# Kernel tuning notes

Hardware: AMD Instinct MI355X
Metric: run time of the kernel (lower is better)

## Reference

```python
import itertools
import jax, jax.numpy as jnp
import numpy as np

B, S, DIM = 1024, 49, 448
KEY_DIM, NUM_HEADS, ATTN_RATIO, RES = 32, 8, 4, 7
EXP_DIM = ATTN_RATIO * KEY_DIM            # 128
TOT_KEY = KEY_DIM * NUM_HEADS             # 256
TOT_EXP = EXP_DIM * NUM_HEADS             # 1024
QKV_OUT = TOT_EXP + 2 * TOT_KEY           # 1536
MLP_HID = 4 * DIM                         # 1792
SCALE = KEY_DIM ** -0.5
LN_EPS = 1e-5


def _build_bias_idxs():
    points = list(itertools.product(range(RES), range(RES)))
    offsets = {}
    idxs = []
    for p1 in points:
        for p2 in points:
            off = (abs(p1[0] - p2[0]), abs(p1[1] - p2[1]))
            if off not in offsets:
                offsets[off] = len(offsets)
            idxs.append(offsets[off])
    return np.array(idxs, dtype=np.int32).reshape(len(points), len(points)), len(offsets)


def setup_inputs() -> dict:
    key = jax.random.key(0)
    ks = jax.random.split(key, 16)
    bias_idxs_np, n_off = _build_bias_idxs()
    sd = 0.02
    return {
        "hidden_states": jax.random.normal(ks[0], (B, S, DIM), jnp.float32),
        "qkv_w": jax.random.normal(ks[1], (DIM, QKV_OUT), jnp.float32) * sd,
        "qkv_b": jnp.zeros((QKV_OUT,), jnp.float32),
        "proj_w": jax.random.normal(ks[2], (TOT_EXP, DIM), jnp.float32) * sd,
        "proj_b": jnp.zeros((DIM,), jnp.float32),
        "ln1_g": jnp.ones((DIM,), jnp.float32),
        "ln1_b": jnp.zeros((DIM,), jnp.float32),
        "ln2_g": jnp.ones((DIM,), jnp.float32),
        "ln2_b": jnp.zeros((DIM,), jnp.float32),
        "mlp_w1": jax.random.normal(ks[3], (DIM, MLP_HID), jnp.float32) * sd,
        "mlp_b1": jnp.zeros((MLP_HID,), jnp.float32),
        "mlp_w2": jax.random.normal(ks[4], (MLP_HID, DIM), jnp.float32) * sd,
        "mlp_b2": jnp.zeros((DIM,), jnp.float32),
        "attn_biases": jax.random.normal(ks[5], (NUM_HEADS, n_off), jnp.float32) * sd,
        "ls1": jax.random.normal(ks[6], (DIM,), jnp.float32) * 0.1,
        "ls2": jax.random.normal(ks[7], (DIM,), jnp.float32) * 0.1,
        "bias_idxs": jnp.asarray(bias_idxs_np),
    }


def _layer_norm(x, g, b):
    mu = jnp.mean(x, axis=-1, keepdims=True)
    var = jnp.mean(jnp.square(x - mu), axis=-1, keepdims=True)
    return (x - mu) * jax.lax.rsqrt(var + LN_EPS) * g + b


def reference(hidden_states, qkv_w, qkv_b, proj_w, proj_b,
              ln1_g, ln1_b, ln2_g, ln2_b,
              mlp_w1, mlp_b1, mlp_w2, mlp_b2,
              attn_biases, ls1, ls2, bias_idxs):
    x = hidden_states
    h = _layer_norm(x, ln1_g, ln1_b)
    qkv = h @ qkv_w + qkv_b                               # [B,S,1536]
    qkv = qkv.reshape(B, S, NUM_HEADS, KEY_DIM * 2 + EXP_DIM)
    q, k, v = jnp.split(qkv, [KEY_DIM, 2 * KEY_DIM], axis=3)
    bias = attn_biases[:, bias_idxs]                      # [H,S,S]
    scores = jnp.einsum('bqhd,bkhd->bhqk', q, k) * SCALE + bias
    probs = jax.nn.softmax(scores, axis=-1)
    ctx = jnp.einsum('bhqk,bkhd->bqhd', probs, v).reshape(B, S, TOT_EXP)
    attn_out = ctx @ proj_w + proj_b                      # [B,S,DIM]
    x = x + ls1 * attn_out
    h2 = _layer_norm(x, ln2_g, ln2_b)
    m = jax.nn.gelu(h2 @ mlp_w1 + mlp_b1, approximate=False) @ mlp_w2 + mlp_b2
    return x + ls2 * m
```

## Files before the change

### kernel.cpp

```cpp
#include <hip/hip_runtime.h>
#include <hip/hip_bf16.h>
#include <cstdint>

typedef unsigned short u16;
typedef __bf16 bf16x8 __attribute__((ext_vector_type(8)));
typedef float f32x4 __attribute__((ext_vector_type(4)));

#define DEV __device__ __forceinline__

static constexpr int BATCH = 1024, SEQ = 49, DIM = 448;
static constexpr int NH = 8, DV = 128;
static constexpr int QKV_N = 1536, MLP_H = 1792;
static constexpr float SCALE = 0.17677669529663687f;

DEV u16 f2bf(float f) {
    uint32_t u = __builtin_bit_cast(uint32_t, f);
    u += 0x7fffu + ((u >> 16) & 1u);
    return (u16)(u >> 16);
}

DEV void gload16(const void* g, void* l) {
    __builtin_amdgcn_global_load_lds(
        (__attribute__((address_space(1))) void*)const_cast<void*>(g),
        (__attribute__((address_space(3))) void*)l, 16, 0, 0);
}

#define MFMA(a, b, c) __builtin_amdgcn_mfma_f32_16x16x32_bf16((a), (b), (c), 0, 0, 0)

__global__ __launch_bounds__(256) void transpose_cast(const float* __restrict__ src,
                                                      u16* __restrict__ dst,
                                                      int K, int N, int Npad) {
    __shared__ float t[32][33];
    int nbk = K >> 5;
    int bk = blockIdx.x % nbk;
    int bn = blockIdx.x / nbk;
    int lx = threadIdx.x & 31, ly = threadIdx.x >> 5;
    int n0 = bn * 32, k0 = bk * 32;
    #pragma unroll
    for (int i = 0; i < 32; i += 8) {
        int k = k0 + ly + i, n = n0 + lx;
        t[ly + i][lx] = (n < N) ? src[(size_t)k * N + n] : 0.f;
    }
    __syncthreads();
    #pragma unroll
    for (int i = 0; i < 32; i += 8) {
        int n = n0 + ly + i, k = k0 + lx;
        dst[(size_t)n * K + k] = f2bf(t[lx][ly + i]);
    }
}

__global__ void build_bias(const float* __restrict__ ab, const int* __restrict__ idxs,
                           float* __restrict__ tab, int n_off) {
    int i = blockIdx.x * 256 + threadIdx.x;
    if (i >= NH * 49 * 49) return;
    int h = i / 2401, rem = i % 2401;
    tab[i] = ab[h * n_off + idxs[rem]];
}

__global__ __launch_bounds__(256) void ln_kernel(const float* __restrict__ x,
                                                 const float* __restrict__ g,
                                                 const float* __restrict__ bb,
                                                 u16* __restrict__ out) {
    int row = blockIdx.x * 4 + (threadIdx.x >> 6);
    int l = threadIdx.x & 63;
    const float* xr = x + (size_t)row * DIM;
    float v[7];
    float s = 0.f;
    #pragma unroll
    for (int j = 0; j < 7; j++) { v[j] = xr[l + j * 64]; s += v[j]; }
    #pragma unroll
    for (int m = 32; m; m >>= 1) s += __shfl_xor(s, m, 64);
    float mu = s * (1.f / 448.f);
    float var = 0.f;
    #pragma unroll
    for (int j = 0; j < 7; j++) { float d = v[j] - mu; var += d * d; }
    #pragma unroll
    for (int m = 32; m; m >>= 1) var += __shfl_xor(var, m, 64);
    float rs = rsqrtf(var * (1.f / 448.f) + 1e-5f);
    u16* orow = out + (size_t)row * DIM;
    #pragma unroll
    for (int j = 0; j < 7; j++) {
        int c = l + j * 64;
        orow[c] = f2bf((v[j] - mu) * rs * g[c] + bb[c]);
    }
}

template <int EPI>
__global__ __launch_bounds__(512, 6) void gemm128(const u16* __restrict__ A,
                                                  const u16* __restrict__ BT,
                                                  int Mreal, int N, int K, int Nreal,
                                                  const float* __restrict__ bias,
                                                  const float* __restrict__ ls,
                                                  const float* __restrict__ xres,
                                                  u16* __restrict__ outB,
                                                  float* __restrict__ outF) {
    __shared__ __align__(16) u16 sa[128 * 64];
    __shared__ __align__(16) u16 sb[128 * 64];
    const int tid = threadIdx.x;
    const int tilesN = N >> 7;

    int bid = blockIdx.x;
    int nwg = gridDim.x;
    if ((nwg & 7) == 0) {
        int cpx = nwg >> 3;
        bid = (bid & 7) * cpx + (bid >> 3);
    }
    const int tm = bid / tilesN, tn = bid % tilesN;

    const int w = tid >> 6, l = tid & 63;
    const int wm = (w >> 2) * 64, wn = (w & 3) * 32;
    const int l15 = l & 15, l4 = l >> 4;

    const u16* gA[2];
    const u16* gB[2];
    int loff[2];
    const size_t baseB = (size_t)(tn * 128) * K;
    #pragma unroll
    for (int i = 0; i < 2; i++) {
        int lc = i * 512 + tid;
        int row = lc >> 3, cs = lc & 7;
        int scs = cs ^ (row & 7);
        int gm = tm * 128 + row;
        gm = gm < Mreal ? gm : Mreal - 1;
        gA[i] = A + (size_t)gm * K + scs * 8;
        gB[i] = BT + baseB + (size_t)row * K + scs * 8;
        loff[i] = (row * 8 + cs) * 8;
    }

    f32x4 acc[4][2];
    #pragma unroll
    for (int i = 0; i < 4; i++)
        #pragma unroll
        for (int j = 0; j < 2; j++) acc[i][j] = (f32x4){0.f, 0.f, 0.f, 0.f};

    const int nk = K >> 6;
    #pragma unroll 1
    for (int kt = 0; kt < nk; ++kt) {
        const int k0 = kt << 6;
        #pragma unroll
        for (int i = 0; i < 2; i++) gload16(gA[i] + k0, &sa[loff[i]]);
        #pragma unroll
        for (int i = 0; i < 2; i++) gload16(gB[i] + k0, &sb[loff[i]]);
        __syncthreads();
        #pragma unroll
        for (int ks = 0; ks < 2; ++ks) {
            bf16x8 af[4], bfr[2];
            #pragma unroll
            for (int i = 0; i < 4; i++) {
                int row = wm + i * 16 + l15;
                int c = (ks * 4 + l4) ^ (row & 7);
                af[i] = *(const bf16x8*)&sa[row * 64 + c * 8];
            }
            #pragma unroll
            for (int j = 0; j < 2; j++) {
                int row = wn + j * 16 + l15;
                int c = (ks * 4 + l4) ^ (row & 7);
                bfr[j] = *(const bf16x8*)&sb[row * 64 + c * 8];
            }
            #pragma unroll
            for (int i = 0; i < 4; i++)
                #pragma unroll
                for (int j = 0; j < 2; j++)
                    acc[i][j] = MFMA(af[i], bfr[j], acc[i][j]);
        }
        __syncthreads();
    }

    #pragma unroll
    for (int i = 0; i < 4; i++) {
        int row0 = tm * 128 + wm + i * 16 + l4 * 4;
        #pragma unroll
        for (int j = 0; j < 2; j++) {
            int col = tn * 128 + wn + j * 16 + l15;
            if (col >= Nreal) continue;
            float bv = bias[col];
            #pragma unroll
            for (int r = 0; r < 4; r++) {
                int m = row0 + r;
                if (m >= Mreal) continue;
                float v = acc[i][j][r] + bv;
                if (EPI == 0) {
                    outB[(size_t)m * Nreal + col] = f2bf(v);
                } else if (EPI == 1) {
                    float gl = 0.5f * v * (1.f + erff(v * 0.70710678118654752f));
                    outB[(size_t)m * Nreal + col] = f2bf(gl);
                } else {
                    outF[(size_t)m * DIM + col] = xres[(size_t)m * DIM + col] + ls[col] * v;
                }
            }
        }
    }
}

__global__ __launch_bounds__(256) void attn_kernel(const u16* __restrict__ qkv,
                                                   const float* __restrict__ btab,
                                                   u16* __restrict__ ctx) {
    __shared__ __align__(16) u16 sq[64 * 40];
    __shared__ __align__(16) u16 sk[64 * 40];
    __shared__ __align__(16) u16 sv[128 * 72];
    __shared__ __align__(16) u16 sp[64 * 72];
    const int tid = threadIdx.x;
    const int bh = blockIdx.x;
    const int b = bh >> 3, h = bh & 7;
    const int w = tid >> 6, l = tid & 63, l15 = l & 15, l4 = l >> 4;
    const f32x4 Z4 = {0.f, 0.f, 0.f, 0.f};
    const size_t rowbase = (size_t)(b * SEQ) * QKV_N + h * 192;

    for (int c = tid; c < SEQ * 4; c += 256) {
        int s = c >> 2, ch = c & 3;
        *(uint4*)&sq[s * 40 + ch * 8] = *(const uint4*)(qkv + rowbase + (size_t)s * QKV_N + ch * 8);
        *(uint4*)&sk[s * 40 + ch * 8] = *(const uint4*)(qkv + rowbase + (size_t)s * QKV_N + 32 + ch * 8);
    }
    for (int c = tid; c < 15 * 5; c += 256) {
        int s = SEQ + c / 5, ch = c % 5;
        *(uint4*)&sq[s * 40 + ch * 8] = (uint4){0, 0, 0, 0};
        *(uint4*)&sk[s * 40 + ch * 8] = (uint4){0, 0, 0, 0};
    }
    for (int c = tid; c < SEQ * 16; c += 256) {
        int s = c >> 4, ch = c & 15;
        uint4 vv = *(const uint4*)(qkv + rowbase + (size_t)s * QKV_N + 64 + ch * 8);
        const u16* pv = (const u16*)&vv;
        #pragma unroll
        for (int j = 0; j < 8; j++) sv[(ch * 8 + j) * 72 + s] = pv[j];
    }
    for (int c = tid; c < 128 * 15; c += 256) {
        int d = c / 15, s = SEQ + c % 15;
        sv[d * 72 + s] = 0;
    }
    __syncthreads();

    bf16x8 aq = *(const bf16x8*)&sq[(w * 16 + l15) * 40 + l4 * 8];
    f32x4 sc[4];
    #pragma unroll
    for (int j = 0; j < 4; j++) {
        bf16x8 bk = *(const bf16x8*)&sk[(j * 16 + l15) * 40 + l4 * 8];
        sc[j] = MFMA(aq, bk, Z4);
    }
    #pragma unroll
    for (int r = 0; r < 4; r++) {
        int row = w * 16 + l4 * 4 + r;
        float pv[4];
        #pragma unroll
        for (int j = 0; j < 4; j++) {
            int col = j * 16 + l15;
            float sval = -1e30f;
            if (row < SEQ && col < SEQ)
                sval = sc[j][r] * SCALE + btab[(h * SEQ + row) * SEQ + col];
            pv[j] = sval;
        }
        float m = fmaxf(fmaxf(pv[0], pv[1]), fmaxf(pv[2], pv[3]));
        #pragma unroll
        for (int mask = 1; mask < 16; mask <<= 1) m = fmaxf(m, __shfl_xor(m, mask, 16));
        float s = 0.f;
        #pragma unroll
        for (int j = 0; j < 4; j++) { pv[j] = expf(pv[j] - m); s += pv[j]; }
        #pragma unroll
        for (int mask = 1; mask < 16; mask <<= 1) s += __shfl_xor(s, mask, 16);
        float inv = 1.f / s;
        #pragma unroll
        for (int j = 0; j < 4; j++) sp[row * 72 + j * 16 + l15] = f2bf(pv[j] * inv);
    }
    __syncthreads();

    bf16x8 ap0 = *(const bf16x8*)&sp[(w * 16 + l15) * 72 + l4 * 8];
    bf16x8 ap1 = *(const bf16x8*)&sp[(w * 16 + l15) * 72 + 32 + l4 * 8];
    #pragma unroll
    for (int j = 0; j < 8; j++) {
        bf16x8 b0 = *(const bf16x8*)&sv[(j * 16 + l15) * 72 + l4 * 8];
        bf16x8 b1 = *(const bf16x8*)&sv[(j * 16 + l15) * 72 + 32 + l4 * 8];
        f32x4 a = MFMA(ap0, b0, Z4);
        a = MFMA(ap1, b1, a);
        #pragma unroll
        for (int r = 0; r < 4; r++) {
            int row = w * 16 + l4 * 4 + r;
            if (row < SEQ)
                ctx[((size_t)(b * SEQ) + row) * 1024 + h * DV + j * 16 + l15] = f2bf(a[r]);
        }
    }
}

extern "C" void kernel_launch(void* const* d_in, const int* in_sizes, int n_in,
                              void* d_out, int out_size, void* d_ws, size_t ws_size,
                              hipStream_t stream) {
    const float* x = (const float*)d_in[0];
    const float* qkv_w = (const float*)d_in[1];
    const float* qkv_b = (const float*)d_in[2];
    const float* proj_w = (const float*)d_in[3];
    const float* proj_b = (const float*)d_in[4];
    const float* ln1_g = (const float*)d_in[5];
    const float* ln1_b = (const float*)d_in[6];
    const float* ln2_g = (const float*)d_in[7];
    const float* ln2_b = (const float*)d_in[8];
    const float* mlp_w1 = (const float*)d_in[9];
    const float* mlp_b1 = (const float*)d_in[10];
    const float* mlp_w2 = (const float*)d_in[11];
    const float* mlp_b2 = (const float*)d_in[12];
    const float* attn_biases = (const float*)d_in[13];
    const float* ls1 = (const float*)d_in[14];
    const float* ls2 = (const float*)d_in[15];
    const int* bias_idxs = (const int*)d_in[16];
    int n_off = in_sizes[13] / NH;
    float* out = (float*)d_out;

    auto al = [](size_t b) { return (b + 255) & ~(size_t)255; };
    const size_t wbytes = al((size_t)QKV_N * DIM * 2) + al((size_t)512 * 1024 * 2) +
                          al((size_t)MLP_H * DIM * 2) + al((size_t)512 * MLP_H * 2) +
                          al((size_t)NH * 2401 * 4);

    int nc = 32;
    {
        const int cands[6] = {1, 2, 4, 8, 16, 32};
        for (int ci = 0; ci < 6; ci++) {
            size_t R = (size_t)(BATCH / cands[ci]) * SEQ;
            size_t need = wbytes + al(R * DIM * 2) + al(R * MLP_H * 2) + al(R * 1024 * 2);
            if (need <= ws_size) { nc = cands[ci]; break; }
        }
    }
    const int CH = BATCH / nc;
    const int R = CH * SEQ;
    const int MT = (R + 127) >> 7;

    char* ws = (char*)d_ws;
    size_t off = 0;
    auto alloc = [&](size_t bytes) {
        void* p = ws + off;
        off += al(bytes);
        return p;
    };
    u16* wt_qkv = (u16*)alloc((size_t)QKV_N * DIM * 2);
    u16* wt_proj = (u16*)alloc((size_t)512 * 1024 * 2);
    u16* wt_m1 = (u16*)alloc((size_t)MLP_H * DIM * 2);
    u16* wt_m2 = (u16*)alloc((size_t)512 * MLP_H * 2);
    float* btab = (float*)alloc((size_t)NH * 2401 * 4);
    u16* hbuf = (u16*)alloc((size_t)R * DIM * 2);
    u16* big = (u16*)alloc((size_t)R * MLP_H * 2);
    u16* ctx = (u16*)alloc((size_t)R * 1024 * 2);

    transpose_cast<<<(DIM / 32) * (QKV_N / 32), 256, 0, stream>>>(qkv_w, wt_qkv, DIM, QKV_N, QKV_N);
    transpose_cast<<<(1024 / 32) * (512 / 32), 256, 0, stream>>>(proj_w, wt_proj, 1024, DIM, 512);
    transpose_cast<<<(DIM / 32) * (MLP_H / 32), 256, 0, stream>>>(mlp_w1, wt_m1, DIM, MLP_H, MLP_H);
    transpose_cast<<<(MLP_H / 32) * (512 / 32), 256, 0, stream>>>(mlp_w2, wt_m2, MLP_H, DIM, 512);
    build_bias<<<(NH * 2401 + 255) / 256, 256, 0, stream>>>(attn_biases, bias_idxs, btab, n_off);

    for (int c = 0; c < nc; ++c) {
        const float* xc = x + (size_t)c * R * DIM;
        float* oc = out + (size_t)c * R * DIM;

        ln_kernel<<<R / 4, 256, 0, stream>>>(xc, ln1_g, ln1_b, hbuf);
        gemm128<0><<<MT * (QKV_N / 128), 512, 0, stream>>>(
            hbuf, wt_qkv, R, QKV_N, DIM, QKV_N, qkv_b, nullptr, nullptr, big, nullptr);
        attn_kernel<<<CH * NH, 256, 0, stream>>>(big, btab, ctx);
        gemm128<2><<<MT * 4, 512, 0, stream>>>(
            ctx, wt_proj, R, 512, 1024, DIM, proj_b, ls1, xc, nullptr, oc);
        ln_kernel<<<R / 4, 256, 0, stream>>>(oc, ln2_g, ln2_b, hbuf);
        gemm128<1><<<MT * (MLP_H / 128), 512, 0, stream>>>(
            hbuf, wt_m1, R, MLP_H, DIM, MLP_H, mlp_b1, nullptr, nullptr, big, nullptr);
        gemm128<2><<<MT * 4, 512, 0, stream>>>(
            big, wt_m2, R, 512, MLP_H, DIM, mlp_b2, ls2, oc, nullptr, oc);
    }
}
```

Measured before the change: 755.2 us.

## Double-buffer GEMM LDS tiles with prefetch two k-steps ahead

Splits the GEMM's shared-memory A/B tiles into two buffers and issues global-to-LDS loads for tile kt+2 while tile kt is being computed, using explicit vmcnt waits and barriers. The aim is to hide global load latency behind MFMA work instead of stalling on a sync every k-step. This doubles LDS use to 64KB per block, and the launch-bounds occupancy hint drops from 6 to 4 blocks.

```diff
diff --git a/kernel.cpp b/kernel.cpp
--- a/kernel.cpp
+++ b/kernel.cpp
@@ -86,7 +86,7 @@
 }
 
 template <int EPI>
-__global__ __launch_bounds__(512, 6) void gemm128(const u16* __restrict__ A,
+__global__ __launch_bounds__(512, 4) void gemm128(const u16* __restrict__ A,
                                                   const u16* __restrict__ BT,
                                                   int Mreal, int N, int K, int Nreal,
                                                   const float* __restrict__ bias,
@@ -94,8 +94,8 @@
                                                   const float* __restrict__ xres,
                                                   u16* __restrict__ outB,
                                                   float* __restrict__ outF) {
-    __shared__ __align__(16) u16 sa[128 * 64];
-    __shared__ __align__(16) u16 sb[128 * 64];
+    __shared__ __align__(16) u16 sa[2][128 * 64];
+    __shared__ __align__(16) u16 sb[2][128 * 64];
     const int tid = threadIdx.x;
     const int tilesN = N >> 7;
 
@@ -127,6 +127,14 @@
         loff[i] = (row * 8 + cs) * 8;
     }
 
+    auto STAGE = [&](int buf, int kt) {
+        const int k0 = kt << 6;
+        #pragma unroll
+        for (int i = 0; i < 2; i++) gload16(gA[i] + k0, &sa[buf][loff[i]]);
+        #pragma unroll
+        for (int i = 0; i < 2; i++) gload16(gB[i] + k0, &sb[buf][loff[i]]);
+    };
+
     f32x4 acc[4][2];
     #pragma unroll
     for (int i = 0; i < 4; i++)
@@ -134,14 +142,15 @@
         for (int j = 0; j < 2; j++) acc[i][j] = (f32x4){0.f, 0.f, 0.f, 0.f};
 
     const int nk = K >> 6;
+    STAGE(0, 0);
+    STAGE(1, 1);
+    asm volatile("s_waitcnt vmcnt(4)" ::: "memory");
+    __builtin_amdgcn_s_barrier();
+    __builtin_amdgcn_sched_barrier(0);
+
+    int cur = 0;
     #pragma unroll 1
     for (int kt = 0; kt < nk; ++kt) {
-        const int k0 = kt << 6;
-        #pragma unroll
-        for (int i = 0; i < 2; i++) gload16(gA[i] + k0, &sa[loff[i]]);
-        #pragma unroll
-        for (int i = 0; i < 2; i++) gload16(gB[i] + k0, &sb[loff[i]]);
-        __syncthreads();
         #pragma unroll
         for (int ks = 0; ks < 2; ++ks) {
             bf16x8 af[4], bfr[2];
@@ -149,13 +158,13 @@
             for (int i = 0; i < 4; i++) {
                 int row = wm + i * 16 + l15;
                 int c = (ks * 4 + l4) ^ (row & 7);
-                af[i] = *(const bf16x8*)&sa[row * 64 + c * 8];
+                af[i] = *(const bf16x8*)&sa[cur][row * 64 + c * 8];
             }
             #pragma unroll
             for (int j = 0; j < 2; j++) {
                 int row = wn + j * 16 + l15;
                 int c = (ks * 4 + l4) ^ (row & 7);
-                bfr[j] = *(const bf16x8*)&sb[row * 64 + c * 8];
+                bfr[j] = *(const bf16x8*)&sb[cur][row * 64 + c * 8];
             }
             #pragma unroll
             for (int i = 0; i < 4; i++)
@@ -163,7 +172,17 @@
                 for (int j = 0; j < 2; j++)
                     acc[i][j] = MFMA(af[i], bfr[j], acc[i][j]);
         }
-        __syncthreads();
+        __builtin_amdgcn_s_barrier();
+        __builtin_amdgcn_sched_barrier(0);
+        if (kt + 2 < nk) {
+            STAGE(cur, kt + 2);
+            asm volatile("s_waitcnt vmcnt(4)" ::: "memory");
+        } else {
+            asm volatile("s_waitcnt vmcnt(0)" ::: "memory");
+        }
+        __builtin_amdgcn_s_barrier();
+        __builtin_amdgcn_sched_barrier(0);
+        cur ^= 1;
     }
 
     #pragma unroll
```

Measured after the change: 847.5 us. +12.2%, slower.
